# Kernel optimization log

Measured on AMD Instinct MI355X. Metric: run time of the kernel, lower is better.

Reference implementation:

```python
import jax, jax.numpy as jnp
import numpy as np
import math

H = 512        # hidden_size (channels)
N = 64         # state_size
MAX_LEN = 4096 # kernel length L
BATCH = 8
SEQ = 4096     # seq len of input (== MAX_LEN here)


def _nplr(n):
    # HiPPO-LegS NPLR decomposition (done once at init, numpy float64 for eig stability)
    i = np.arange(n, dtype=np.float64)
    j = np.sqrt(2 * i + 1)
    A = -(np.tril(j[None, :] * j[:, None]) - np.diag(i))
    Bv = j.astype(np.complex128)
    p = j / np.sqrt(2.0)
    w, V = np.linalg.eig(A + p[None, :] * p[:, None])  # normal part; conj-pair eigvals adjacent
    w = w[::2].copy()          # [N/2]
    V = V[:, ::2].copy()       # [N, N/2]
    Bc = V.conj().T @ Bv       # [N/2]
    pc = V.conj().T @ p.astype(np.complex128)
    V_full = np.concatenate([V, V.conj()], axis=-1)      # [N, N]
    VtAV = V_full.conj().T @ A.astype(np.complex128) @ V_full  # [N, N]
    return w, pc, V, Bc, VtAV


def _ri(c):
    # complex -> trailing real/imag pair, float32 (mirrors torch.view_as_real)
    return np.stack([c.real, c.imag], axis=-1).astype(np.float32)


def setup_inputs() -> dict:
    rng = np.random.default_rng(0)
    w, p, V, Bc, Amat = _nplr(N)
    Brep = np.tile(Bc[None, :], (H, 1))                      # [H, N/2]
    C = rng.standard_normal((H, N)).astype(np.complex128)
    C = C @ V.conj()                                         # einsum('hn,nm->hm') -> [H, N/2]
    log_dt = math.log(1e-3) + (math.log(1e-1) - math.log(1e-3)) * rng.random(H)
    dt = np.exp(log_dt)[:, None, None]
    I = np.eye(N, dtype=np.complex128)[None]
    dA = np.linalg.inv(I - dt * Amat / 2) @ (I + dt * Amat / 2)   # [H, N, N]
    dA_power = I - np.linalg.matrix_power(dA, MAX_LEN)
    C2 = np.concatenate([C, C.conj()], axis=-1)              # [H, N]
    C2 = np.einsum('hmn,hm->hn', dA_power.conj(), C2)[:, : N // 2]
    p_rep = np.tile(p[None, None, :], (H, 1, 1))             # [H, 1, N/2]
    Bfull = np.concatenate([Brep[:, None, :], p_rep], axis=1)  # [H, 2, N/2]
    Cfull = np.concatenate([C2[:, None, :], p_rep], axis=1)    # [H, 2, N/2] (q == p)

    key = jax.random.key(0)
    kx, kd = jax.random.split(key)
    return {
        "x": jax.random.normal(kx, (BATCH, SEQ, H), dtype=jnp.float32),
        "log_dt": jnp.asarray(log_dt, dtype=jnp.float32),   # [H]
        "w_ri": jnp.asarray(_ri(w)),                        # [N/2, 2]
        "B_ri": jnp.asarray(_ri(Bfull)),                    # [H, 2, N/2, 2]
        "C_ri": jnp.asarray(_ri(Cfull)),                    # [H, 2, N/2, 2]
        "D": jax.random.normal(kd, (H,), dtype=jnp.float32),
    }


def _s4_kernel(log_dt, w_ri, B_ri, C_ri):
    L = MAX_LEN
    w = w_ri[..., 0] + 1j * w_ri[..., 1]   # [n] with n = N/2
    B = B_ri[..., 0] + 1j * B_ri[..., 1]   # [H, 2, n]
    C = C_ri[..., 0] + 1j * C_ri[..., 1]   # [H, 2, n]
    dt = jnp.exp(log_dt)                   # [H]
    freq = jnp.exp(-2j * jnp.pi / L * jnp.arange(L // 2 + 1))  # [F], F = L/2+1
    z = 2 * (1 - freq) / (1 + freq)        # bilinear-transformed frequencies

    v = C[:, :, None, :].conj() * B[:, None, :, :]   # [H, 2, 2, n]
    wd = w[None, :] * dt[:, None]                    # [H, n]
    # cauchy_mult: r = sum_n v/(z-w) + conj(v)/(z-conj(w)), as batched matmuls over n
    K1 = 1.0 / (z[None, None, :] - wd[:, :, None])          # [H, n, F]
    K2 = 1.0 / (z[None, None, :] - wd.conj()[:, :, None])   # [H, n, F]
    r = jnp.einsum('habn,hnf->habf', v, K1) + jnp.einsum('habn,hnf->habf', v.conj(), K2)
    r = r * dt[:, None, None, None]
    # Woodbury correction for the rank-1 (p, q) augmentation
    k_f = r[:, 0, 0, :] - r[:, 0, 1, :] * r[:, 1, 0, :] / (1 + r[:, 1, 1, :])  # [H, F]
    k_f = k_f * 2 / (1 + freq)
    return jnp.fft.irfft(k_f)   # [H, L]


def reference(x, log_dt, w_ri, B_ri, C_ri, D):
    k = _s4_kernel(log_dt, w_ri, B_ri, C_ri)     # [H, L]
    xt = jnp.transpose(x, (0, 2, 1))             # [B, H, Lx]
    L2 = 2 * MAX_LEN                              # conv pads to 2*kernel_len
    k_f = jnp.fft.rfft(k, n=L2)                  # [H, L2/2+1]
    x_f = jnp.fft.rfft(xt, n=L2)                 # [B, H, L2/2+1]
    y = jnp.fft.irfft(k_f[None] * x_f, n=L2)[..., : xt.shape[-1]]
    y = y + xt * D[None, :, None]                # skip connection
    return jnp.transpose(y, (0, 2, 1))           # [B, Lx, H]
```

## Files before the change

kernel.cpp:

```cpp
#include <hip/hip_runtime.h>
#include <math.h>

#define TPB 256
#define CTPB 512

__device__ __forceinline__ float2 cmul(float2 a, float2 b) {
    return make_float2(a.x * b.x - a.y * b.y, a.x * b.y + a.y * b.x);
}
__device__ __forceinline__ float2 cmulc(float2 a, float2 b) {
    return make_float2(a.x * b.x + a.y * b.y, a.x * b.y - a.y * b.x);
}
__device__ __forceinline__ float2 cdivf(float2 a, float2 b) {
    float inv = 1.0f / (b.x * b.x + b.y * b.y);
    return make_float2((a.x * b.x + a.y * b.y) * inv, (a.y * b.x - a.x * b.y) * inv);
}
__device__ __forceinline__ float2 cadd(float2 a, float2 b) { return make_float2(a.x + b.x, a.y + b.y); }
__device__ __forceinline__ float2 csub(float2 a, float2 b) { return make_float2(a.x - b.x, a.y - b.y); }
__device__ __forceinline__ float2 mul_i(float2 a, float d) {
    return make_float2(-d * a.y, d * a.x);
}
__device__ __forceinline__ int brev11(int x) { return (int)(__brev((unsigned)x) >> 21); }
__device__ __forceinline__ int rev8(int x) {
    return ((x & 7) << 9) | (((x >> 3) & 7) << 6) | (((x >> 6) & 7) << 3) | ((x >> 9) & 7);
}
__device__ __forceinline__ int swz(int i) { return i ^ ((i >> 4) & 15) ^ ((i >> 8) & 15); }

__device__ __forceinline__ void dft8(const float2* x, float2* y, float d) {
    const float r = 0.70710678118f;
    float2 s0 = cadd(x[0], x[4]), t0 = csub(x[0], x[4]);
    float2 s1 = cadd(x[1], x[5]), t1 = csub(x[1], x[5]);
    float2 s2 = cadd(x[2], x[6]), t2 = csub(x[2], x[6]);
    float2 s3 = cadd(x[3], x[7]), t3 = csub(x[3], x[7]);
    t1 = cmul(t1, make_float2(r, d * r));
    t2 = mul_i(t2, d);
    t3 = cmul(t3, make_float2(-r, d * r));
    float2 u0 = cadd(s0, s2), v0 = csub(s0, s2);
    float2 u1 = cadd(s1, s3), v1 = mul_i(csub(s1, s3), d);
    y[0] = cadd(u0, u1); y[4] = csub(u0, u1);
    y[2] = cadd(v0, v1); y[6] = csub(v0, v1);
    float2 p0 = cadd(t0, t2), q0 = csub(t0, t2);
    float2 p1 = cadd(t1, t3), q1 = mul_i(csub(t1, t3), d);
    y[1] = cadd(p0, p1); y[5] = csub(p0, p1);
    y[3] = cadd(q0, q1); y[7] = csub(q0, q1);
}

template <int LOGN, int NT>
__device__ void fft8_dif(float2* s, int tid, float dir) {
    const int N = 1 << LOGN;
#pragma unroll
    for (int hb = LOGN - 3; hb >= 0; hb -= 3) {
        const int h = 1 << hb;
        const float astep = dir * 6.283185307179586f / (float)(h << 3);
        __syncthreads();
#pragma unroll
        for (int it = 0; it < (N >> 3) / NT; ++it) {
            const int b = tid + it * NT;
            int j = b & (h - 1);
            int base = ((b >> hb) << (hb + 3)) + j;
            int s0 = swz(base);
            float2 x[8];
#pragma unroll
            for (int k = 0; k < 8; ++k) x[k] = s[s0 ^ swz(k << hb)];
            float2 y[8];
            dft8(x, y, dir);
            float ang = astep * (float)j;
            float c, sn;
            __sincosf(ang, &sn, &c);
            float2 w = make_float2(c, sn), wm = w;
            s[s0] = y[0];
#pragma unroll
            for (int m = 1; m < 8; ++m) {
                s[s0 ^ swz(m << hb)] = cmul(wm, y[m]);
                wm = cmul(wm, w);
            }
        }
    }
    __syncthreads();
}

template <int LOGN, int NT>
__device__ void fft8_dit(float2* s, int tid, float dir) {
    const int N = 1 << LOGN;
#pragma unroll
    for (int hb = 0; hb < LOGN; hb += 3) {
        const int h = 1 << hb;
        const float astep = dir * 6.283185307179586f / (float)(h << 3);
        __syncthreads();
#pragma unroll
        for (int it = 0; it < (N >> 3) / NT; ++it) {
            const int b = tid + it * NT;
            int j = b & (h - 1);
            int base = ((b >> hb) << (hb + 3)) + j;
            int s0 = swz(base);
            float ang = astep * (float)j;
            float c, sn;
            __sincosf(ang, &sn, &c);
            float2 w = make_float2(c, sn);
            float2 x[8];
            x[0] = s[s0];
            float2 wm = w;
#pragma unroll
            for (int k = 1; k < 8; ++k) {
                x[k] = cmul(wm, s[s0 ^ swz(k << hb)]);
                wm = cmul(wm, w);
            }
            float2 y[8];
            dft8(x, y, dir);
#pragma unroll
            for (int m = 0; m < 8; ++m) s[s0 ^ swz(m << hb)] = y[m];
        }
    }
    __syncthreads();
}

template <int LOGN>
__device__ void fft_dif2(float2* s, int tid, float dir) {
    const int N = 1 << LOGN;
    for (int st = LOGN - 1; st >= 0; --st) {
        __syncthreads();
        int half = 1 << st;
        for (int b = tid; b < (N >> 1); b += TPB) {
            int j  = b & (half - 1);
            int i0 = ((b >> st) << (st + 1)) + j;
            int i1 = i0 + half;
            float2 u = s[i0], v = s[i1];
            float ang = dir * 3.14159265358979f * (float)j / (float)half;
            float c, sn;
            __sincosf(ang, &sn, &c);
            float2 d = make_float2(u.x - v.x, u.y - v.y);
            s[i0] = make_float2(u.x + v.x, u.y + v.y);
            s[i1] = cmul(make_float2(c, sn), d);
        }
    }
    __syncthreads();
}

__global__ __launch_bounds__(TPB) void kf_kernel(
    const float* __restrict__ log_dt, const float* __restrict__ w_ri,
    const float* __restrict__ Bri, const float* __restrict__ Cri,
    float2* __restrict__ kf) {
    __shared__ float2 wds[32];
    __shared__ float aab[4][32], rab[4][32];
    __shared__ float qn[32], pn[32];
    const int h   = blockIdx.x;
    const int tid = threadIdx.x;
    const float dt = expf(log_dt[h]);
    if (tid < 32) {
        float wr = w_ri[2 * tid] * dt, wi = w_ri[2 * tid + 1] * dt;
        wds[tid] = make_float2(wr, wi);
        qn[tid]  = wr * wr + wi * wi;
        pn[tid]  = -2.0f * wr;
    }
    __syncthreads();
    if (tid < 128) {
        int a = tid >> 6, b = (tid >> 5) & 1, n = tid & 31;
        const float* Cp = Cri + (((h * 2 + a) * 32) + n) * 2;
        const float* Bp = Bri + (((h * 2 + b) * 32) + n) * 2;
        float Cr = Cp[0], Ci = Cp[1], Br = Bp[0], Bi = Bp[1];
        float2 v = make_float2(Cr * Br + Ci * Bi, Cr * Bi - Ci * Br);
        float2 wd = wds[n];
        aab[a * 2 + b][n] = -2.0f * (v.x * wd.x + v.y * wd.y);
        rab[a * 2 + b][n] = 2.0f * v.x;
    }
    __syncthreads();
    const int by   = blockIdx.y;
    const int fend = (by == 3) ? 2049 : (by + 1) * 512;
    for (int f = by * 512 + tid; f < fend; f += TPB) {
        float th = (6.283185307179586f / 4096.0f) * (float)f;
        float cf = cosf(th), sf = sinf(th);
        float2 den = make_float2(1.0f + cf, -sf);
        float zt  = 2.0f * tanf(0.5f * th);
        float zt2 = zt * zt;
        float2 r00 = make_float2(0.f, 0.f), r01 = r00, r10 = r00, r11 = r00;
        for (int n = 0; n < 32; ++n) {
            float c   = qn[n] - zt2;
            float d   = pn[n] * zt;
            float inv = 1.0f / (c * c + d * d);
            float cc = c * inv, dd = d * inv;
            float a0 = aab[0][n], b0 = rab[0][n] * zt;
            r00.x += a0 * cc + b0 * dd; r00.y += b0 * cc - a0 * dd;
            float a1 = aab[1][n], b1 = rab[1][n] * zt;
            r01.x += a1 * cc + b1 * dd; r01.y += b1 * cc - a1 * dd;
            float a2 = aab[2][n], b2 = rab[2][n] * zt;
            r10.x += a2 * cc + b2 * dd; r10.y += b2 * cc - a2 * dd;
            float a3 = aab[3][n], b3 = rab[3][n] * zt;
            r11.x += a3 * cc + b3 * dd; r11.y += b3 * cc - a3 * dd;
        }
        r00.x *= dt; r00.y *= dt; r01.x *= dt; r01.y *= dt;
        r10.x *= dt; r10.y *= dt; r11.x *= dt; r11.y *= dt;
        float2 q  = cdivf(cmul(r01, r10), make_float2(1.0f + r11.x, r11.y));
        float2 k0 = make_float2(r00.x - q.x, r00.y - q.y);
        float2 kv = cmul(k0, cdivf(make_float2(2.0f, 0.0f), den));
        kf[h * 2049 + f] = kv;
    }
}

__global__ __launch_bounds__(TPB) void kprep_kernel(const float2* __restrict__ kf,
                                                    float2* __restrict__ Kt) {
    __shared__ float2 s[4096];
    const int hh = blockIdx.x, tid = threadIdx.x;
    const float2* X = kf + hh * 2049;
    for (int m = tid; m < 2048; m += TPB) {
        float2 Xm = X[m];
        float2 Xc = X[2048 - m];
        if (m == 0) { Xm.y = 0.0f; Xc.y = 0.0f; }
        float2 A  = make_float2(Xm.x + Xc.x, Xm.y - Xc.y);
        float2 Bv = make_float2(Xm.x - Xc.x, Xm.y + Xc.y);
        float ang = (3.14159265358979f / 2048.0f) * (float)m;
        float c, sn;
        __sincosf(ang, &sn, &c);
        float2 O = cmul(make_float2(c, sn), Bv);
        s[m] = make_float2(0.5f * (A.x - O.y), 0.5f * (A.y + O.x));
    }
    fft_dif2<11>(s, tid, +1.0f);
    float2 reg[8];
    const float sc = 1.0f / 2048.0f;
#pragma unroll
    for (int i = 0; i < 8; ++i) {
        int t = tid + TPB * i;
        float2 v = s[brev11(t)];
        reg[i] = make_float2(v.x * sc, v.y * sc);
    }
    __syncthreads();
#pragma unroll
    for (int i = 0; i < 8; ++i) {
        int t = tid + TPB * i;
        s[swz(t)]        = reg[i];
        s[swz(t + 2048)] = make_float2(0.f, 0.f);
    }
    fft8_dif<12, TPB>(s, tid, -1.0f);
    float2* K = Kt + (size_t)hh * 4097;
    for (int p = tid; p < 4096; p += TPB) {
        int j  = rev8(p);
        int jc = (4096 - j) & 4095;
        int pc = rev8(jc);
        float2 Yj = s[swz(p)], Yc = s[swz(pc)];
        float2 A  = make_float2(Yj.x + Yc.x, Yj.y - Yc.y);
        float2 Bv = make_float2(Yj.x - Yc.x, Yj.y + Yc.y);
        float ang = -(3.14159265358979f / 4096.0f) * (float)j;
        float c, sn;
        __sincosf(ang, &sn, &c);
        float2 t2 = cmul(make_float2(c, sn), make_float2(Bv.y, -Bv.x));
        K[p] = make_float2(0.5f * (A.x + t2.x), 0.5f * (A.y + t2.y));
        if (p == 0) K[4096] = make_float2(Yj.x - Yj.y, 0.0f);
    }
}

__global__ __launch_bounds__(TPB) void transpose_in(const float* __restrict__ x,
                                                    float* __restrict__ xt) {
    __shared__ float tile[64][65];
    const int b = blockIdx.z, t0 = blockIdx.y * 64, h0 = blockIdx.x * 64;
    const int tid = threadIdx.x;
    const float4* xv = (const float4*)(x + ((size_t)b * 4096 + t0) * 512 + h0);
#pragma unroll
    for (int i = 0; i < 4; ++i) {
        int idx = tid + TPB * i;
        int tl = idx >> 4, hq = idx & 15;
        float4 v = xv[(size_t)tl * 128 + hq];
        tile[tl][hq * 4 + 0] = v.x; tile[tl][hq * 4 + 1] = v.y;
        tile[tl][hq * 4 + 2] = v.z; tile[tl][hq * 4 + 3] = v.w;
    }
    __syncthreads();
    float* xo = xt + ((size_t)(b * 512 + h0)) * 4096 + t0;
#pragma unroll
    for (int i = 0; i < 4; ++i) {
        int idx = tid + TPB * i;
        int hl = idx >> 4, tq = idx & 15;
        float4 v = make_float4(tile[tq * 4 + 0][hl], tile[tq * 4 + 1][hl],
                               tile[tq * 4 + 2][hl], tile[tq * 4 + 3][hl]);
        ((float4*)(xo + (size_t)hl * 4096))[tq] = v;
    }
}

__global__ __launch_bounds__(CTPB) void conv_kernel(const float* xt,
                                                    const float2* __restrict__ Kt,
                                                    float* yt) {
    __shared__ float2 s[4096];
    const int row = blockIdx.x, tid = threadIdx.x;
    const int hch = row & 511;
    const int stid = swz(tid);
    const float2* xr = (const float2*)(xt + (size_t)row * 4096);
#pragma unroll
    for (int i = 0; i < 8; ++i) {
        int t = tid + CTPB * i;
        s[stid ^ swz(CTPB * i)] = (t < 2048) ? xr[t] : make_float2(0.f, 0.f);
    }
    fft8_dif<12, CTPB>(s, tid, -1.0f);
    const float2* K = Kt + (size_t)hch * 4097;
#pragma unroll
    for (int i = 0; i < 8; ++i) {
        int p  = tid + CTPB * i;
        int sp = stid ^ swz(CTPB * i);
        if (p == 0) {
            float2 Y0 = s[sp];
            float X0 = Y0.x + Y0.y;
            float Xn = Y0.x - Y0.y;
            float Z0 = X0 * K[0].x;
            float Zn = Xn * K[4096].x;
            s[sp] = make_float2(0.5f * (Z0 + Zn), 0.5f * (Z0 - Zn));
            continue;
        }
        int j  = rev8(p);
        int jc = 4096 - j;
        int pc = rev8(jc & 4095);
        if (pc < p) continue;
        float2 Yj = s[sp], Yc = s[swz(pc)];
        float2 A  = make_float2(Yj.x + Yc.x, Yj.y - Yc.y);
        float2 Bv = make_float2(Yj.x - Yc.x, Yj.y + Yc.y);
        float ang = -(3.14159265358979f / 4096.0f) * (float)j;
        float c, sn;
        __sincosf(ang, &sn, &c);
        float2 W = make_float2(c, sn);
        float2 t2 = cmul(W, make_float2(Bv.y, -Bv.x));
        float2 Xj = make_float2(0.5f * (A.x + t2.x), 0.5f * (A.y + t2.y));
        float2 t2c = cmul(make_float2(-W.x, W.y), make_float2(Bv.y, Bv.x));
        float2 Xc2 = make_float2(0.5f * (A.x + t2c.x), 0.5f * (-A.y + t2c.y));
        float2 Zj = cmul(Xj, K[p]);
        float2 Zc = cmul(Xc2, K[pc]);
        float2 A2 = make_float2(Zj.x + Zc.x, Zj.y - Zc.y);
        float2 B2 = make_float2(Zj.x - Zc.x, Zj.y + Zc.y);
        float2 O2 = cmul(make_float2(W.x, -W.y), B2);
        s[sp] = make_float2(0.5f * (A2.x - O2.y), 0.5f * (A2.y + O2.x));
        if (pc != p) {
            float2 O2c = cmul(make_float2(-W.x, -W.y), make_float2(-B2.x, B2.y));
            s[swz(pc)] = make_float2(0.5f * (A2.x - O2c.y), 0.5f * (-A2.y + O2c.x));
        }
    }
    fft8_dit<12, CTPB>(s, tid, +1.0f);
    float2* yo = (float2*)(yt + (size_t)row * 4096);
    const float sc = 1.0f / 4096.0f;
#pragma unroll
    for (int i = 0; i < 4; ++i) {
        int t = tid + CTPB * i;
        float2 y = s[stid ^ swz(CTPB * i)];
        yo[t] = make_float2(y.x * sc, y.y * sc);
    }
}

__global__ __launch_bounds__(TPB) void transpose_out(const float* __restrict__ yt,
                                                     const float* __restrict__ x,
                                                     const float* __restrict__ Dv,
                                                     float* __restrict__ out) {
    __shared__ float tile[64][65];
    const int b = blockIdx.z, t0 = blockIdx.y * 64, h0 = blockIdx.x * 64;
    const int tid = threadIdx.x;
    const float* yp = yt + ((size_t)(b * 512 + h0)) * 4096 + t0;
#pragma unroll
    for (int i = 0; i < 4; ++i) {
        int idx = tid + TPB * i;
        int hl = idx >> 4, tq = idx & 15;
        float4 v = ((const float4*)(yp + (size_t)hl * 4096))[tq];
        tile[tq * 4 + 0][hl] = v.x; tile[tq * 4 + 1][hl] = v.y;
        tile[tq * 4 + 2][hl] = v.z; tile[tq * 4 + 3][hl] = v.w;
    }
    __syncthreads();
    const float4* xv = (const float4*)(x + ((size_t)b * 4096 + t0) * 512 + h0);
    float4* ov = (float4*)(out + ((size_t)b * 4096 + t0) * 512 + h0);
    const float4* D4 = (const float4*)(Dv + h0);
#pragma unroll
    for (int i = 0; i < 4; ++i) {
        int idx = tid + TPB * i;
        int tl = idx >> 4, hq = idx & 15;
        float4 xvv = xv[(size_t)tl * 128 + hq];
        float4 d = D4[hq];
        float4 v = make_float4(tile[tl][4 * hq + 0] + d.x * xvv.x,
                               tile[tl][4 * hq + 1] + d.y * xvv.y,
                               tile[tl][4 * hq + 2] + d.z * xvv.z,
                               tile[tl][4 * hq + 3] + d.w * xvv.w);
        ov[(size_t)tl * 128 + hq] = v;
    }
}

extern "C" void kernel_launch(void* const* d_in, const int* in_sizes, int n_in,
                              void* d_out, int out_size, void* d_ws, size_t ws_size,
                              hipStream_t stream) {
    (void)in_sizes; (void)n_in; (void)out_size; (void)ws_size;
    const float* x      = (const float*)d_in[0];
    const float* log_dt = (const float*)d_in[1];
    const float* w_ri   = (const float*)d_in[2];
    const float* Bri    = (const float*)d_in[3];
    const float* Cri    = (const float*)d_in[4];
    const float* Dv     = (const float*)d_in[5];
    float* out = (float*)d_out;

    char* ws = (char*)d_ws;
    float*  xt = (float*)(ws);
    float2* kf = (float2*)(ws + 67108864);
    float2* Kt = (float2*)(ws + 75501568);

    kf_kernel<<<dim3(512, 4), TPB, 0, stream>>>(log_dt, w_ri, Bri, Cri, kf);
    kprep_kernel<<<512, TPB, 0, stream>>>(kf, Kt);
    transpose_in<<<dim3(8, 64, 8), TPB, 0, stream>>>(x, xt);
    conv_kernel<<<4096, CTPB, 0, stream>>>(xt, Kt, xt);
    transpose_out<<<dim3(8, 64, 8), TPB, 0, stream>>>(xt, x, Dv, out);
}
```

Baseline: 303.1 us.

## Fuse skip connection into conv and prune zero-padded FFT stages

The first DIF stage of the conv FFT is specialised to exploit zero padding: it loads the four nonzero inputs directly from global memory into registers. The last DIT stage computes only the needed low half of outputs and adds the D*x skip term there, so transpose_out no longer reads x. Unit-twiddle stages skip sincos, and kprep uses 512 threads. This cuts shared-memory passes and global traffic, at the cost of an extra read of xt in the conv epilogue.

```diff
diff --git a/kernel.cpp b/kernel.cpp
--- a/kernel.cpp
+++ b/kernel.cpp
@@ -3,12 +3,10 @@
 
 #define TPB 256
 #define CTPB 512
+#define KTPB 512
 
 __device__ __forceinline__ float2 cmul(float2 a, float2 b) {
     return make_float2(a.x * b.x - a.y * b.y, a.x * b.y + a.y * b.x);
-}
-__device__ __forceinline__ float2 cmulc(float2 a, float2 b) {
-    return make_float2(a.x * b.x + a.y * b.y, a.x * b.y - a.y * b.x);
 }
 __device__ __forceinline__ float2 cdivf(float2 a, float2 b) {
     float inv = 1.0f / (b.x * b.x + b.y * b.y);
@@ -44,6 +42,100 @@
     y[3] = cadd(q0, q1); y[7] = csub(q0, q1);
 }
 
+__device__ __forceinline__ void dft8z(float2 x0, float2 x1, float2 x2, float2 x3,
+                                      float2* y, float d) {
+    const float r = 0.70710678118f;
+    float2 u0 = cadd(x0, x2), v0 = csub(x0, x2);
+    float2 u1 = cadd(x1, x3), v1 = mul_i(csub(x1, x3), d);
+    float2 t1 = cmul(x1, make_float2(r, d * r));
+    float2 t2 = mul_i(x2, d);
+    float2 t3 = cmul(x3, make_float2(-r, d * r));
+    float2 p0 = cadd(x0, t2), q0 = csub(x0, t2);
+    float2 p1 = cadd(t1, t3), q1 = mul_i(csub(t1, t3), d);
+    y[0] = cadd(u0, u1); y[4] = csub(u0, u1);
+    y[2] = cadd(v0, v1); y[6] = csub(v0, v1);
+    y[1] = cadd(p0, p1); y[5] = csub(p0, p1);
+    y[3] = cadd(q0, q1); y[7] = csub(q0, q1);
+}
+
+__device__ __forceinline__ void dft8_lo(const float2* x, float2* y, float d) {
+    const float r = 0.70710678118f;
+    float2 s0 = cadd(x[0], x[4]), t0 = csub(x[0], x[4]);
+    float2 s1 = cadd(x[1], x[5]), t1 = csub(x[1], x[5]);
+    float2 s2 = cadd(x[2], x[6]), t2 = csub(x[2], x[6]);
+    float2 s3 = cadd(x[3], x[7]), t3 = csub(x[3], x[7]);
+    t1 = cmul(t1, make_float2(r, d * r));
+    t2 = mul_i(t2, d);
+    t3 = cmul(t3, make_float2(-r, d * r));
+    float2 u0 = cadd(s0, s2), v0 = csub(s0, s2);
+    float2 u1 = cadd(s1, s3), v1 = mul_i(csub(s1, s3), d);
+    y[0] = cadd(u0, u1);
+    y[2] = cadd(v0, v1);
+    float2 p0 = cadd(t0, t2), q0 = csub(t0, t2);
+    float2 p1 = cadd(t1, t3), q1 = mul_i(csub(t1, t3), d);
+    y[1] = cadd(p0, p1);
+    y[3] = cadd(q0, q1);
+}
+
+template <int HB, int DIR>
+__device__ __forceinline__ void dif_stage(float2* s, int tid) {
+    __syncthreads();
+    const int h = 1 << HB;
+    int j = tid & (h - 1);
+    int base = ((tid >> HB) << (HB + 3)) + j;
+    int s0 = swz(base);
+    float2 x[8];
+#pragma unroll
+    for (int k = 0; k < 8; ++k) x[k] = s[s0 ^ swz(k << HB)];
+    float2 y[8];
+    dft8(x, y, (float)DIR);
+    if constexpr (HB != 0) {
+        float ang = (float)DIR * 6.283185307179586f / (float)(h << 3) * (float)j;
+        float c, sn;
+        __sincosf(ang, &sn, &c);
+        float2 w = make_float2(c, sn), wm = w;
+        s[s0] = y[0];
+#pragma unroll
+        for (int m = 1; m < 8; ++m) {
+            s[s0 ^ swz(m << HB)] = cmul(wm, y[m]);
+            wm = cmul(wm, w);
+        }
+    } else {
+#pragma unroll
+        for (int m = 0; m < 8; ++m) s[s0 ^ swz(m << HB)] = y[m];
+    }
+}
+
+template <int HB, int DIR>
+__device__ __forceinline__ void dit_stage(float2* s, int tid) {
+    __syncthreads();
+    const int h = 1 << HB;
+    int j = tid & (h - 1);
+    int base = ((tid >> HB) << (HB + 3)) + j;
+    int s0 = swz(base);
+    float2 x[8];
+    if constexpr (HB != 0) {
+        float ang = (float)DIR * 6.283185307179586f / (float)(h << 3) * (float)j;
+        float c, sn;
+        __sincosf(ang, &sn, &c);
+        float2 w = make_float2(c, sn);
+        x[0] = s[s0];
+        float2 wm = w;
+#pragma unroll
+        for (int k = 1; k < 8; ++k) {
+            x[k] = cmul(wm, s[s0 ^ swz(k << HB)]);
+            wm = cmul(wm, w);
+        }
+    } else {
+#pragma unroll
+        for (int k = 0; k < 8; ++k) x[k] = s[s0 ^ swz(k << HB)];
+    }
+    float2 y[8];
+    dft8(x, y, (float)DIR);
+#pragma unroll
+    for (int m = 0; m < 8; ++m) s[s0 ^ swz(m << HB)] = y[m];
+}
+
 template <int LOGN, int NT>
 __device__ void fft8_dif(float2* s, int tid, float dir) {
     const int N = 1 << LOGN;
@@ -63,15 +155,20 @@
             for (int k = 0; k < 8; ++k) x[k] = s[s0 ^ swz(k << hb)];
             float2 y[8];
             dft8(x, y, dir);
-            float ang = astep * (float)j;
-            float c, sn;
-            __sincosf(ang, &sn, &c);
-            float2 w = make_float2(c, sn), wm = w;
-            s[s0] = y[0];
-#pragma unroll
-            for (int m = 1; m < 8; ++m) {
-                s[s0 ^ swz(m << hb)] = cmul(wm, y[m]);
-                wm = cmul(wm, w);
+            if (hb != 0) {
+                float ang = astep * (float)j;
+                float c, sn;
+                __sincosf(ang, &sn, &c);
+                float2 w = make_float2(c, sn), wm = w;
+                s[s0] = y[0];
+#pragma unroll
+                for (int m = 1; m < 8; ++m) {
+                    s[s0 ^ swz(m << hb)] = cmul(wm, y[m]);
+                    wm = cmul(wm, w);
+                }
+            } else {
+#pragma unroll
+                for (int m = 0; m < 8; ++m) s[s0 ^ swz(m << hb)] = y[m];
             }
         }
     }
@@ -79,57 +176,26 @@
 }
 
 template <int LOGN, int NT>
-__device__ void fft8_dit(float2* s, int tid, float dir) {
-    const int N = 1 << LOGN;
-#pragma unroll
-    for (int hb = 0; hb < LOGN; hb += 3) {
-        const int h = 1 << hb;
-        const float astep = dir * 6.283185307179586f / (float)(h << 3);
-        __syncthreads();
-#pragma unroll
-        for (int it = 0; it < (N >> 3) / NT; ++it) {
-            const int b = tid + it * NT;
-            int j = b & (h - 1);
-            int base = ((b >> hb) << (hb + 3)) + j;
-            int s0 = swz(base);
-            float ang = astep * (float)j;
-            float c, sn;
-            __sincosf(ang, &sn, &c);
-            float2 w = make_float2(c, sn);
-            float2 x[8];
-            x[0] = s[s0];
-            float2 wm = w;
-#pragma unroll
-            for (int k = 1; k < 8; ++k) {
-                x[k] = cmul(wm, s[s0 ^ swz(k << hb)]);
-                wm = cmul(wm, w);
-            }
-            float2 y[8];
-            dft8(x, y, dir);
-#pragma unroll
-            for (int m = 0; m < 8; ++m) s[s0 ^ swz(m << hb)] = y[m];
-        }
-    }
-    __syncthreads();
-}
-
-template <int LOGN>
 __device__ void fft_dif2(float2* s, int tid, float dir) {
     const int N = 1 << LOGN;
     for (int st = LOGN - 1; st >= 0; --st) {
         __syncthreads();
         int half = 1 << st;
-        for (int b = tid; b < (N >> 1); b += TPB) {
+        for (int b = tid; b < (N >> 1); b += NT) {
             int j  = b & (half - 1);
             int i0 = ((b >> st) << (st + 1)) + j;
             int i1 = i0 + half;
             float2 u = s[i0], v = s[i1];
-            float ang = dir * 3.14159265358979f * (float)j / (float)half;
-            float c, sn;
-            __sincosf(ang, &sn, &c);
             float2 d = make_float2(u.x - v.x, u.y - v.y);
             s[i0] = make_float2(u.x + v.x, u.y + v.y);
-            s[i1] = cmul(make_float2(c, sn), d);
+            if (half > 1) {
+                float ang = dir * 3.14159265358979f * (float)j / (float)half;
+                float c, sn;
+                __sincosf(ang, &sn, &c);
+                s[i1] = cmul(make_float2(c, sn), d);
+            } else {
+                s[i1] = d;
+            }
         }
     }
     __syncthreads();
@@ -195,12 +261,12 @@
     }
 }
 
-__global__ __launch_bounds__(TPB) void kprep_kernel(const float2* __restrict__ kf,
-                                                    float2* __restrict__ Kt) {
+__global__ __launch_bounds__(KTPB) void kprep_kernel(const float2* __restrict__ kf,
+                                                     float2* __restrict__ Kt) {
     __shared__ float2 s[4096];
     const int hh = blockIdx.x, tid = threadIdx.x;
     const float2* X = kf + hh * 2049;
-    for (int m = tid; m < 2048; m += TPB) {
+    for (int m = tid; m < 2048; m += KTPB) {
         float2 Xm = X[m];
         float2 Xc = X[2048 - m];
         if (m == 0) { Xm.y = 0.0f; Xc.y = 0.0f; }
@@ -212,25 +278,25 @@
         float2 O = cmul(make_float2(c, sn), Bv);
         s[m] = make_float2(0.5f * (A.x - O.y), 0.5f * (A.y + O.x));
     }
-    fft_dif2<11>(s, tid, +1.0f);
-    float2 reg[8];
+    fft_dif2<11, KTPB>(s, tid, +1.0f);
+    float2 reg[4];
     const float sc = 1.0f / 2048.0f;
 #pragma unroll
-    for (int i = 0; i < 8; ++i) {
-        int t = tid + TPB * i;
+    for (int i = 0; i < 4; ++i) {
+        int t = tid + KTPB * i;
         float2 v = s[brev11(t)];
         reg[i] = make_float2(v.x * sc, v.y * sc);
     }
     __syncthreads();
 #pragma unroll
-    for (int i = 0; i < 8; ++i) {
-        int t = tid + TPB * i;
+    for (int i = 0; i < 4; ++i) {
+        int t = tid + KTPB * i;
         s[swz(t)]        = reg[i];
         s[swz(t + 2048)] = make_float2(0.f, 0.f);
     }
-    fft8_dif<12, TPB>(s, tid, -1.0f);
+    fft8_dif<12, KTPB>(s, tid, -1.0f);
     float2* K = Kt + (size_t)hh * 4097;
-    for (int p = tid; p < 4096; p += TPB) {
+    for (int p = tid; p < 4096; p += KTPB) {
         int j  = rev8(p);
         int jc = (4096 - j) & 4095;
         int pc = rev8(jc);
@@ -274,18 +340,33 @@
 
 __global__ __launch_bounds__(CTPB) void conv_kernel(const float* xt,
                                                     const float2* __restrict__ Kt,
+                                                    const float* __restrict__ Dv,
                                                     float* yt) {
     __shared__ float2 s[4096];
     const int row = blockIdx.x, tid = threadIdx.x;
     const int hch = row & 511;
     const int stid = swz(tid);
     const float2* xr = (const float2*)(xt + (size_t)row * 4096);
-#pragma unroll
-    for (int i = 0; i < 8; ++i) {
-        int t = tid + CTPB * i;
-        s[stid ^ swz(CTPB * i)] = (t < 2048) ? xr[t] : make_float2(0.f, 0.f);
-    }
-    fft8_dif<12, CTPB>(s, tid, -1.0f);
+
+    {
+        float2 x0 = xr[tid], x1 = xr[tid + 512], x2 = xr[tid + 1024], x3 = xr[tid + 1536];
+        float2 y[8];
+        dft8z(x0, x1, x2, x3, y, -1.0f);
+        float ang = -(6.283185307179586f / 4096.0f) * (float)tid;
+        float c, sn;
+        __sincosf(ang, &sn, &c);
+        float2 w = make_float2(c, sn), wm = w;
+        s[stid] = y[0];
+#pragma unroll
+        for (int m = 1; m < 8; ++m) {
+            s[stid ^ swz(m << 9)] = cmul(wm, y[m]);
+            wm = cmul(wm, w);
+        }
+    }
+    dif_stage<6, -1>(s, tid);
+    dif_stage<3, -1>(s, tid);
+    dif_stage<0, -1>(s, tid);
+    __syncthreads();
     const float2* K = Kt + (size_t)hch * 4097;
 #pragma unroll
     for (int i = 0; i < 8; ++i) {
@@ -326,20 +407,38 @@
             s[swz(pc)] = make_float2(0.5f * (A2.x - O2c.y), 0.5f * (-A2.y + O2c.x));
         }
     }
-    fft8_dit<12, CTPB>(s, tid, +1.0f);
-    float2* yo = (float2*)(yt + (size_t)row * 4096);
-    const float sc = 1.0f / 4096.0f;
-#pragma unroll
-    for (int i = 0; i < 4; ++i) {
-        int t = tid + CTPB * i;
-        float2 y = s[stid ^ swz(CTPB * i)];
-        yo[t] = make_float2(y.x * sc, y.y * sc);
+    dit_stage<0, 1>(s, tid);
+    dit_stage<3, 1>(s, tid);
+    dit_stage<6, 1>(s, tid);
+    __syncthreads();
+    {
+        float ang = (6.283185307179586f / 4096.0f) * (float)tid;
+        float c, sn;
+        __sincosf(ang, &sn, &c);
+        float2 w = make_float2(c, sn);
+        float2 x[8];
+        x[0] = s[stid];
+        float2 wm = w;
+#pragma unroll
+        for (int k = 1; k < 8; ++k) {
+            x[k] = cmul(wm, s[stid ^ swz(k << 9)]);
+            wm = cmul(wm, w);
+        }
+        float2 y[4];
+        dft8_lo(x, y, 1.0f);
+        const float D = Dv[hch];
+        float2* yo = (float2*)(yt + (size_t)row * 4096);
+        const float sc = 1.0f / 4096.0f;
+#pragma unroll
+        for (int m = 0; m < 4; ++m) {
+            int t2 = tid + (m << 9);
+            float2 xin = xr[t2];
+            yo[t2] = make_float2(y[m].x * sc + D * xin.x, y[m].y * sc + D * xin.y);
+        }
     }
 }
 
 __global__ __launch_bounds__(TPB) void transpose_out(const float* __restrict__ yt,
-                                                     const float* __restrict__ x,
-                                                     const float* __restrict__ Dv,
                                                      float* __restrict__ out) {
     __shared__ float tile[64][65];
     const int b = blockIdx.z, t0 = blockIdx.y * 64, h0 = blockIdx.x * 64;
@@ -354,19 +453,13 @@
         tile[tq * 4 + 2][hl] = v.z; tile[tq * 4 + 3][hl] = v.w;
     }
     __syncthreads();
-    const float4* xv = (const float4*)(x + ((size_t)b * 4096 + t0) * 512 + h0);
     float4* ov = (float4*)(out + ((size_t)b * 4096 + t0) * 512 + h0);
-    const float4* D4 = (const float4*)(Dv + h0);
 #pragma unroll
     for (int i = 0; i < 4; ++i) {
         int idx = tid + TPB * i;
         int tl = idx >> 4, hq = idx & 15;
-        float4 xvv = xv[(size_t)tl * 128 + hq];
-        float4 d = D4[hq];
-        float4 v = make_float4(tile[tl][4 * hq + 0] + d.x * xvv.x,
-                               tile[tl][4 * hq + 1] + d.y * xvv.y,
-                               tile[tl][4 * hq + 2] + d.z * xvv.z,
-                               tile[tl][4 * hq + 3] + d.w * xvv.w);
+        float4 v = make_float4(tile[tl][4 * hq + 0], tile[tl][4 * hq + 1],
+                               tile[tl][4 * hq + 2], tile[tl][4 * hq + 3]);
         ov[(size_t)tl * 128 + hq] = v;
     }
 }
@@ -389,8 +482,8 @@
     float2* Kt = (float2*)(ws + 75501568);
 
     kf_kernel<<<dim3(512, 4), TPB, 0, stream>>>(log_dt, w_ri, Bri, Cri, kf);
-    kprep_kernel<<<512, TPB, 0, stream>>>(kf, Kt);
+    kprep_kernel<<<512, KTPB, 0, stream>>>(kf, Kt);
     transpose_in<<<dim3(8, 64, 8), TPB, 0, stream>>>(x, xt);
-    conv_kernel<<<4096, CTPB, 0, stream>>>(xt, Kt, xt);
-    transpose_out<<<dim3(8, 64, 8), TPB, 0, stream>>>(xt, x, Dv, out);
-}
+    conv_kernel<<<4096, CTPB, 0, stream>>>(xt, Kt, Dv, xt);
+    transpose_out<<<dim3(8, 64, 8), TPB, 0, stream>>>(xt, out);
+}
```

After: 282.6 us. 1.07x faster.
